# Kernel tuning notes

Measured on AMD Instinct MI355X. Metric: run time of the kernel, lower is better.

## Reference

```python
import jax, jax.numpy as jnp
import numpy as np

D_POINTS, D_MODEL, K, B, N = 64, 128, 16, 2, 16384


def _linear(x, w, b=None):
    y = x @ w.T
    return y if b is None else y + b


def setup_inputs() -> dict:
    key = jax.random.key(0)
    ks = jax.random.split(key, 16)
    s = 0.02
    inp = {
        "new_xyz": jax.random.normal(ks[0], (B, N, 3), jnp.float32),
        "grouped_xyz": jax.random.normal(ks[1], (B, 3, N, K), jnp.float32),
        "grouped_idx": jax.random.randint(ks[2], (B, N, K), 0, N),
        "features": jax.random.normal(ks[3], (B, N, D_POINTS), jnp.float32),
        "fc1_w": jax.random.normal(ks[4], (D_MODEL, D_POINTS), jnp.float32) * s,
        "fc1_b": jnp.zeros((D_MODEL,), jnp.float32),
        "wq": jax.random.normal(ks[5], (D_MODEL, D_MODEL), jnp.float32) * s,
        "wk": jax.random.normal(ks[6], (D_MODEL, D_MODEL), jnp.float32) * s,
        "wv": jax.random.normal(ks[7], (D_MODEL, D_MODEL), jnp.float32) * s,
        "delta_w1": jax.random.normal(ks[8], (D_MODEL, 3), jnp.float32) * s,
        "delta_b1": jnp.zeros((D_MODEL,), jnp.float32),
        "delta_w2": jax.random.normal(ks[9], (D_MODEL, D_MODEL), jnp.float32) * s,
        "delta_b2": jnp.zeros((D_MODEL,), jnp.float32),
        "gamma_w1": jax.random.normal(ks[10], (D_MODEL, D_MODEL), jnp.float32) * s,
        "gamma_b1": jnp.zeros((D_MODEL,), jnp.float32),
        "gamma_w2": jax.random.normal(ks[11], (D_MODEL, D_MODEL), jnp.float32) * s,
        "gamma_b2": jnp.zeros((D_MODEL,), jnp.float32),
    }
    return inp


def reference(new_xyz, grouped_xyz, grouped_idx, features,
              fc1_w, fc1_b, wq, wk, wv,
              delta_w1, delta_b1, delta_w2, delta_b2,
              gamma_w1, gamma_b1, gamma_w2, gamma_b2):
    # x: [B,N,d_model]
    x = _linear(features, fc1_w, fc1_b)
    q = x @ wq.T                               # [B,N,d]
    kx = x @ wk.T                              # [B,N,d]
    vx = x @ wv.T                              # [B,N,d]
    gather = jax.vmap(lambda a, i: a[i])       # per-batch gather -> [B,N,K,d]
    k = gather(kx, grouped_idx)
    v = gather(vx, grouped_idx)
    # pos_enc: fc_delta(new_xyz[:,:,None] - grouped_xyz.permute(0,2,3,1))
    rel = new_xyz[:, :, None, :] - jnp.transpose(grouped_xyz, (0, 2, 3, 1))  # [B,N,K,3]
    pos_enc = _linear(jax.nn.relu(_linear(rel, delta_w1, delta_b1)), delta_w2, delta_b2)
    # attn: fc_gamma(q - k + pos_enc), softmax over neighbor axis
    h = q[:, :, None, :] - k + pos_enc
    attn = _linear(jax.nn.relu(_linear(h, gamma_w1, gamma_b1)), gamma_w2, gamma_b2)
    attn = jax.nn.softmax(attn / np.sqrt(D_MODEL).astype(np.float32), axis=-2)
    out = jnp.einsum('bmnf,bmnf->bmf', attn, v + pos_enc)
    return out
```

## Files before the change

kernel.cpp:

```cpp
#include <hip/hip_runtime.h>
#include <hip/hip_bf16.h>
#include <math.h>

#define BB   2
#define NPTS 16384
#define KNB  16
#define DPTS 64
#define DM   128

typedef float  f32x4  __attribute__((ext_vector_type(4)));
typedef short  bf16x8 __attribute__((ext_vector_type(8)));

__device__ __forceinline__ unsigned short f2bf(float f) {
    union { __hip_bfloat16 h; unsigned short u; } v;
    v.h = __float2bfloat16(f);
    return v.u;
}
__device__ __forceinline__ float bf2f(unsigned short h) {
    union { unsigned u; float f; } v; v.u = ((unsigned)h) << 16;
    return v.f;
}

__device__ __forceinline__ int swz(int row, int col) {
    return row * DM + (col ^ ((row & 7) << 3));
}

#define WOFF_DW2  0
#define WOFF_GW1  16384
#define WOFF_GW2  32768
#define WOFF_WQ   49152
#define WOFF_WK   65536
#define WOFF_WV   81920
#define WOFF_FC1  98304
#define WTOT      106496

__global__ __launch_bounds__(256) void cvtw_kernel(
    const float* __restrict__ dw2, const float* __restrict__ gw1,
    const float* __restrict__ gw2, const float* __restrict__ wq,
    const float* __restrict__ wk, const float* __restrict__ wv,
    const float* __restrict__ fc1_w, unsigned short* __restrict__ wb)
{
    const int i = blockIdx.x * 256 + threadIdx.x;
    if (i >= WTOT) return;
    float v;
    if (i < WOFF_WQ) {
        const int which = i >> 14, off = i & 16383;
        v = (which == 0) ? dw2[off] : (which == 1) ? gw1[off] : gw2[off];
    } else if (i < WOFF_FC1) {
        const int j = i - WOFF_WQ;
        const int which = j >> 14, off = j & 16383;
        v = (which == 0) ? wq[off] : (which == 1) ? wk[off] : wv[off];
    } else {
        v = fc1_w[i - WOFF_FC1];
    }
    wb[i] = f2bf(v);
}

__device__ __forceinline__ void mfma_gemm(const unsigned short* __restrict__ AB,
                                          const unsigned short* __restrict__ Wb,
                                          int lane, int wbase, f32x4 acc[4][2])
{
    const int c = lane & 15, g = lane >> 4;
    bf16x8 Bf[2][4];
#pragma unroll
    for (int ct = 0; ct < 2; ++ct)
#pragma unroll
        for (int ks = 0; ks < 4; ++ks)
            Bf[ct][ks] = *(const bf16x8*)&Wb[(wbase + ct * 16 + c) * DM + ks * 32 + g * 8];
#pragma unroll
    for (int rt = 0; rt < 4; ++rt) {
        bf16x8 Af[4];
#pragma unroll
        for (int ks = 0; ks < 4; ++ks)
            Af[ks] = *(const bf16x8*)&AB[swz(rt * 16 + c, ks * 32 + g * 8)];
#pragma unroll
        for (int ct = 0; ct < 2; ++ct)
#pragma unroll
            for (int ks = 0; ks < 4; ++ks)
                acc[rt][ct] = __builtin_amdgcn_mfma_f32_16x16x32_bf16(
                    Af[ks], Bf[ct][ks], acc[rt][ct], 0, 0, 0);
    }
}

#define P_MT  64
#define FSTR  72

__global__ __launch_bounds__(256, 4) void proj_kernel(
    const float* __restrict__ features, const float* __restrict__ fc1_b,
    const unsigned short* __restrict__ wbf,
    unsigned short* __restrict__ qws, unsigned short* __restrict__ kws,
    unsigned short* __restrict__ vws)
{
    __shared__ __align__(16) unsigned short FB[P_MT * FSTR];
    __shared__ __align__(16) unsigned short XB[P_MT * DM];

    const int tid  = threadIdx.x;
    const int lane = tid & 63;
    const int wave = tid >> 6;
    const int wbase = wave * 32;
    const int c  = lane & 15;
    const int g  = lane >> 4;
    const int g4 = g * 4;
    const size_t gp0 = (size_t)blockIdx.x * P_MT;

    for (int i = tid; i < P_MT * 8; i += 256) {
        const int r = i >> 3, o = i & 7;
        const float4 a = *(const float4*)&features[(gp0 + r) * DPTS + o * 8];
        const float4 b = *(const float4*)&features[(gp0 + r) * DPTS + o * 8 + 4];
        bf16x8 t;
        t[0] = (short)f2bf(a.x); t[1] = (short)f2bf(a.y);
        t[2] = (short)f2bf(a.z); t[3] = (short)f2bf(a.w);
        t[4] = (short)f2bf(b.x); t[5] = (short)f2bf(b.y);
        t[6] = (short)f2bf(b.z); t[7] = (short)f2bf(b.w);
        *(bf16x8*)&FB[r * FSTR + o * 8] = t;
    }
    __syncthreads();

    {
        const unsigned short* fw = wbf + WOFF_FC1;
        const float b0 = fc1_b[wbase + c], b1 = fc1_b[wbase + 16 + c];
        f32x4 acc[4][2];
#pragma unroll
        for (int rt = 0; rt < 4; ++rt) {
            acc[rt][0] = (f32x4)b0;
            acc[rt][1] = (f32x4)b1;
        }
        bf16x8 Bf[2][2];
#pragma unroll
        for (int ct = 0; ct < 2; ++ct)
#pragma unroll
            for (int ks = 0; ks < 2; ++ks)
                Bf[ct][ks] = *(const bf16x8*)&fw[(wbase + ct * 16 + c) * DPTS + ks * 32 + g * 8];
#pragma unroll
        for (int rt = 0; rt < 4; ++rt) {
            bf16x8 Af[2];
#pragma unroll
            for (int ks = 0; ks < 2; ++ks)
                Af[ks] = *(const bf16x8*)&FB[(rt * 16 + c) * FSTR + ks * 32 + g * 8];
#pragma unroll
            for (int ct = 0; ct < 2; ++ct)
#pragma unroll
                for (int ks = 0; ks < 2; ++ks)
                    acc[rt][ct] = __builtin_amdgcn_mfma_f32_16x16x32_bf16(
                        Af[ks], Bf[ct][ks], acc[rt][ct], 0, 0, 0);
        }
#pragma unroll
        for (int ct = 0; ct < 2; ++ct) {
            const int col = wbase + ct * 16 + c;
#pragma unroll
            for (int rt = 0; rt < 4; ++rt)
#pragma unroll
                for (int rg = 0; rg < 4; ++rg)
                    XB[swz(rt * 16 + g4 + rg, col)] = f2bf(acc[rt][ct][rg]);
        }
    }
    __syncthreads();

    const unsigned short* wmat[3] = { wbf + WOFF_WQ, wbf + WOFF_WK, wbf + WOFF_WV };
    unsigned short* outp[3] = { qws, kws, vws };
#pragma unroll
    for (int m = 0; m < 3; ++m) {
        f32x4 acc[4][2];
#pragma unroll
        for (int rt = 0; rt < 4; ++rt)
#pragma unroll
            for (int ct = 0; ct < 2; ++ct) acc[rt][ct] = (f32x4)0.f;
        mfma_gemm(XB, wmat[m], lane, wbase, acc);
#pragma unroll
        for (int ct = 0; ct < 2; ++ct) {
            const int col = wbase + ct * 16 + c;
#pragma unroll
            for (int rt = 0; rt < 4; ++rt)
#pragma unroll
                for (int rg = 0; rg < 4; ++rg)
                    outp[m][(gp0 + rt * 16 + g4 + rg) * DM + col] = f2bf(acc[rt][ct][rg]);
        }
    }
}

#define K2_PTS 4
#define K2_R   (K2_PTS * KNB)

__global__ __launch_bounds__(256, 4) void attn_kernel(
    const float* __restrict__ new_xyz, const float* __restrict__ grouped_xyz,
    const int* __restrict__ grouped_idx,
    const float* __restrict__ dw1, const float* __restrict__ db1,
    const float* __restrict__ db2,
    const float* __restrict__ gb1, const float* __restrict__ gb2,
    const unsigned short* __restrict__ wbf,
    const unsigned short* __restrict__ qws, const unsigned short* __restrict__ kws,
    const unsigned short* __restrict__ vws,
    float* __restrict__ out)
{
    __shared__ __align__(16) unsigned short AB[K2_R * DM];
    __shared__ __align__(16) unsigned short SB[K2_R * DM];
    __shared__ float REL[K2_R * 3];
    __shared__ int   IDX[K2_R];

    const int tid  = threadIdx.x;
    const int lane = tid & 63;
    const int wave = tid >> 6;
    const int wbase = wave * 32;
    const int c  = lane & 15;
    const int g  = lane >> 4;
    const int g4 = g * 4;
    const int rr = tid >> 4;
    const int o8 = (tid & 15) * 8;

    const int b   = blockIdx.x / (NPTS / K2_PTS);
    const int m0  = (blockIdx.x % (NPTS / K2_PTS)) * K2_PTS;
    const size_t gp0 = (size_t)b * NPTS + m0;
    const size_t bN  = (size_t)b * NPTS;
    const float SCL = 0.12751743342f;

    const unsigned short* dw2b = wbf + WOFF_DW2;
    const unsigned short* gw1b = wbf + WOFF_GW1;
    const unsigned short* gw2b = wbf + WOFF_GW2;

    float wr[24], bbv[8];
    {
        const float4* wsrc = (const float4*)&dw1[o8 * 3];
#pragma unroll
        for (int t = 0; t < 6; ++t) ((float4*)wr)[t] = wsrc[t];
        const float4* bsrc = (const float4*)&db1[o8];
        ((float4*)bbv)[0] = bsrc[0];
        ((float4*)bbv)[1] = bsrc[1];
    }

    if (tid < K2_R) {
        const int p = tid >> 4, j = tid & 15;
        const size_t m = gp0 + p;
        const int mi = m0 + p;
        IDX[tid] = grouped_idx[m * KNB + j];
#pragma unroll
        for (int cc = 0; cc < 3; ++cc)
            REL[tid * 3 + cc] = new_xyz[m * 3 + cc]
                              - grouped_xyz[(((size_t)b * 3 + cc) * NPTS + mi) * KNB + j];
    }
    __syncthreads();

    bf16x8 q8[4], k8[4];
#pragma unroll
    for (int it = 0; it < 4; ++it) {
        const int r = it * 16 + rr;
        q8[it] = *(const bf16x8*)&qws[(gp0 + it) * DM + o8];
        k8[it] = *(const bf16x8*)&kws[(bN + IDX[r]) * DM + o8];
    }

#pragma unroll
    for (int it = 0; it < 4; ++it) {
        const int r = it * 16 + rr;
        const float rx = REL[r * 3 + 0], ry = REL[r * 3 + 1], rz = REL[r * 3 + 2];
        bf16x8 t;
#pragma unroll
        for (int j = 0; j < 8; ++j) {
            float v = bbv[j];
            v = fmaf(rx, wr[j * 3 + 0], v);
            v = fmaf(ry, wr[j * 3 + 1], v);
            v = fmaf(rz, wr[j * 3 + 2], v);
            t[j] = (short)f2bf(fmaxf(v, 0.f));
        }
        *(bf16x8*)&AB[swz(r, o8)] = t;
    }
    __syncthreads();

    f32x4 posr[4][2];
    {
        const float b0 = db2[wbase + c], b1 = db2[wbase + 16 + c];
#pragma unroll
        for (int rt = 0; rt < 4; ++rt) {
            posr[rt][0] = (f32x4)b0;
            posr[rt][1] = (f32x4)b1;
        }
        mfma_gemm(AB, dw2b, lane, wbase, posr);
#pragma unroll
        for (int ct = 0; ct < 2; ++ct) {
            const int col = wbase + ct * 16 + c;
#pragma unroll
            for (int rt = 0; rt < 4; ++rt)
#pragma unroll
                for (int rg = 0; rg < 4; ++rg)
                    SB[swz(rt * 16 + g4 + rg, col)] = f2bf(posr[rt][ct][rg]);
        }
    }
    __syncthreads();

#pragma unroll
    for (int it = 0; it < 4; ++it) {
        const int r = it * 16 + rr;
        const bf16x8 p8 = *(const bf16x8*)&SB[swz(r, o8)];
        bf16x8 t;
#pragma unroll
        for (int j = 0; j < 8; ++j) {
            const float hv = bf2f((unsigned short)q8[it][j])
                           - bf2f((unsigned short)k8[it][j])
                           + bf2f((unsigned short)p8[j]);
            t[j] = (short)f2bf(hv);
        }
        *(bf16x8*)&AB[swz(r, o8)] = t;
    }
    __syncthreads();

    {
        f32x4 acc[4][2];
        const float b0 = gb1[wbase + c], b1 = gb1[wbase + 16 + c];
#pragma unroll
        for (int rt = 0; rt < 4; ++rt) {
            acc[rt][0] = (f32x4)b0;
            acc[rt][1] = (f32x4)b1;
        }
        mfma_gemm(AB, gw1b, lane, wbase, acc);
#pragma unroll
        for (int ct = 0; ct < 2; ++ct) {
            const int col = wbase + ct * 16 + c;
#pragma unroll
            for (int rt = 0; rt < 4; ++rt)
#pragma unroll
                for (int rg = 0; rg < 4; ++rg)
                    SB[swz(rt * 16 + g4 + rg, col)] = f2bf(fmaxf(acc[rt][ct][rg], 0.f));
        }
    }
    __syncthreads();

    f32x4 lg[4][2];
#pragma unroll
    for (int rt = 0; rt < 4; ++rt)
#pragma unroll
        for (int ct = 0; ct < 2; ++ct) lg[rt][ct] = (f32x4)0.f;
    mfma_gemm(SB, gw2b, lane, wbase, lg);
#pragma unroll
    for (int ct = 0; ct < 2; ++ct) {
        const int col = wbase + ct * 16 + c;
        const float bb = gb2[col];
#pragma unroll
        for (int rt = 0; rt < 4; ++rt)
#pragma unroll
            for (int rg = 0; rg < 4; ++rg)
                lg[rt][ct][rg] = (lg[rt][ct][rg] + bb) * SCL;
    }

#pragma unroll
    for (int rt = 0; rt < 4; ++rt)
#pragma unroll
    for (int ct = 0; ct < 2; ++ct) {
        const int col = wbase + ct * 16 + c;
        f32x4 l = lg[rt][ct];
        float mx = fmaxf(fmaxf(l[0], l[1]), fmaxf(l[2], l[3]));
        mx = fmaxf(mx, __shfl_xor(mx, 16));
        mx = fmaxf(mx, __shfl_xor(mx, 32));
        f32x4 e;
        e[0] = __builtin_amdgcn_exp2f(l[0] - mx);
        e[1] = __builtin_amdgcn_exp2f(l[1] - mx);
        e[2] = __builtin_amdgcn_exp2f(l[2] - mx);
        e[3] = __builtin_amdgcn_exp2f(l[3] - mx);
        float s = e[0] + e[1] + e[2] + e[3];
        s += __shfl_xor(s, 16);
        s += __shfl_xor(s, 32);
        float o = 0.f;
#pragma unroll
        for (int rg = 0; rg < 4; ++rg) {
            const int row = rt * 16 + g4 + rg;
            const float vv = bf2f(vws[(bN + IDX[row]) * DM + col]) + posr[rt][ct][rg];
            o = fmaf(e[rg], vv, o);
        }
        o += __shfl_xor(o, 16);
        o += __shfl_xor(o, 32);
        if (g == 0)
            out[(gp0 + rt) * DM + col] = o * __builtin_amdgcn_rcpf(s);
    }
}

extern "C" void kernel_launch(void* const* d_in, const int* in_sizes, int n_in,
                              void* d_out, int out_size, void* d_ws, size_t ws_size,
                              hipStream_t stream)
{
    const float* new_xyz     = (const float*)d_in[0];
    const float* grouped_xyz = (const float*)d_in[1];
    const int*   grouped_idx = (const int*)d_in[2];
    const float* features    = (const float*)d_in[3];
    const float* fc1_w = (const float*)d_in[4];
    const float* fc1_b = (const float*)d_in[5];
    const float* wq    = (const float*)d_in[6];
    const float* wk    = (const float*)d_in[7];
    const float* wv    = (const float*)d_in[8];
    const float* dw1   = (const float*)d_in[9];
    const float* db1   = (const float*)d_in[10];
    const float* dw2   = (const float*)d_in[11];
    const float* db2   = (const float*)d_in[12];
    const float* gw1   = (const float*)d_in[13];
    const float* gb1   = (const float*)d_in[14];
    const float* gw2   = (const float*)d_in[15];
    const float* gb2   = (const float*)d_in[16];
    float* out = (float*)d_out;

    unsigned short* ws = (unsigned short*)d_ws;
    const size_t npt = (size_t)BB * NPTS * DM;
    unsigned short* qws = ws;
    unsigned short* kws = ws + npt;
    unsigned short* vws = ws + 2 * npt;
    unsigned short* wbf = ws + 3 * npt;

    cvtw_kernel<<<(WTOT + 255) / 256, 256, 0, stream>>>(
        dw2, gw1, gw2, wq, wk, wv, fc1_w, wbf);

    proj_kernel<<<(BB * NPTS) / P_MT, 256, 0, stream>>>(
        features, fc1_b, wbf, qws, kws, vws);

    attn_kernel<<<(BB * NPTS) / K2_PTS, 256, 0, stream>>>(
        new_xyz, grouped_xyz, grouped_idx,
        dw1, db1, db2, gb1, gb2,
        wbf, qws, kws, vws, out);
}
```

Before: 163.0 us.

## Interleave K/V rows and share one LDS buffer to raise attention occupancy

K and V projections are now stored interleaved per point (row stride 2*DM), so the gathered K and V rows for a neighbor index sit next to each other in memory and may share cache lines and DRAM pages. The attention kernel folds its two 16KB LDS staging buffers into one, adding extra barriers before each in-place overwrite. Launch bounds are raised from 4 to 8 blocks per SM to allow more concurrent blocks. The tighter bound may force register spilling, and the added syncs serialize the GEMM phases more.

```diff
diff --git a/kernel.cpp b/kernel.cpp
--- a/kernel.cpp
+++ b/kernel.cpp
@@ -88,8 +88,7 @@
 __global__ __launch_bounds__(256, 4) void proj_kernel(
     const float* __restrict__ features, const float* __restrict__ fc1_b,
     const unsigned short* __restrict__ wbf,
-    unsigned short* __restrict__ qws, unsigned short* __restrict__ kws,
-    unsigned short* __restrict__ vws)
+    unsigned short* __restrict__ qws, unsigned short* __restrict__ kvws)
 {
     __shared__ __align__(16) unsigned short FB[P_MT * FSTR];
     __shared__ __align__(16) unsigned short XB[P_MT * DM];
@@ -157,7 +156,6 @@
     __syncthreads();
 
     const unsigned short* wmat[3] = { wbf + WOFF_WQ, wbf + WOFF_WK, wbf + WOFF_WV };
-    unsigned short* outp[3] = { qws, kws, vws };
 #pragma unroll
     for (int m = 0; m < 3; ++m) {
         f32x4 acc[4][2];
@@ -172,8 +170,13 @@
 #pragma unroll
             for (int rt = 0; rt < 4; ++rt)
 #pragma unroll
-                for (int rg = 0; rg < 4; ++rg)
-                    outp[m][(gp0 + rt * 16 + g4 + rg) * DM + col] = f2bf(acc[rt][ct][rg]);
+                for (int rg = 0; rg < 4; ++rg) {
+                    const size_t row = gp0 + rt * 16 + g4 + rg;
+                    unsigned short* dst = (m == 0)
+                        ? &qws[row * DM + col]
+                        : &kvws[row * (2 * DM) + (m == 2 ? DM : 0) + col];
+                    *dst = f2bf(acc[rt][ct][rg]);
+                }
         }
     }
 }
@@ -181,19 +184,17 @@
 #define K2_PTS 4
 #define K2_R   (K2_PTS * KNB)
 
-__global__ __launch_bounds__(256, 4) void attn_kernel(
+__global__ __launch_bounds__(256, 8) void attn_kernel(
     const float* __restrict__ new_xyz, const float* __restrict__ grouped_xyz,
     const int* __restrict__ grouped_idx,
     const float* __restrict__ dw1, const float* __restrict__ db1,
     const float* __restrict__ db2,
     const float* __restrict__ gb1, const float* __restrict__ gb2,
     const unsigned short* __restrict__ wbf,
-    const unsigned short* __restrict__ qws, const unsigned short* __restrict__ kws,
-    const unsigned short* __restrict__ vws,
+    const unsigned short* __restrict__ qws, const unsigned short* __restrict__ kvws,
     float* __restrict__ out)
 {
-    __shared__ __align__(16) unsigned short AB[K2_R * DM];
-    __shared__ __align__(16) unsigned short SB[K2_R * DM];
+    __shared__ __align__(16) unsigned short X[K2_R * DM];
     __shared__ float REL[K2_R * 3];
     __shared__ int   IDX[K2_R];
 
@@ -244,7 +245,7 @@
     for (int it = 0; it < 4; ++it) {
         const int r = it * 16 + rr;
         q8[it] = *(const bf16x8*)&qws[(gp0 + it) * DM + o8];
-        k8[it] = *(const bf16x8*)&kws[(bN + IDX[r]) * DM + o8];
+        k8[it] = *(const bf16x8*)&kvws[(bN + IDX[r]) * (2 * DM) + o8];
     }
 
 #pragma unroll
@@ -260,7 +261,7 @@
             v = fmaf(rz, wr[j * 3 + 2], v);
             t[j] = (short)f2bf(fmaxf(v, 0.f));
         }
-        *(bf16x8*)&AB[swz(r, o8)] = t;
+        *(bf16x8*)&X[swz(r, o8)] = t;
     }
     __syncthreads();
 
@@ -272,23 +273,24 @@
             posr[rt][0] = (f32x4)b0;
             posr[rt][1] = (f32x4)b1;
         }
-        mfma_gemm(AB, dw2b, lane, wbase, posr);
-#pragma unroll
-        for (int ct = 0; ct < 2; ++ct) {
-            const int col = wbase + ct * 16 + c;
-#pragma unroll
-            for (int rt = 0; rt < 4; ++rt)
-#pragma unroll
-                for (int rg = 0; rg < 4; ++rg)
-                    SB[swz(rt * 16 + g4 + rg, col)] = f2bf(posr[rt][ct][rg]);
-        }
+    }
+    mfma_gemm(X, dw2b, lane, wbase, posr);
+    __syncthreads();
+#pragma unroll
+    for (int ct = 0; ct < 2; ++ct) {
+        const int col = wbase + ct * 16 + c;
+#pragma unroll
+        for (int rt = 0; rt < 4; ++rt)
+#pragma unroll
+            for (int rg = 0; rg < 4; ++rg)
+                X[swz(rt * 16 + g4 + rg, col)] = f2bf(posr[rt][ct][rg]);
     }
     __syncthreads();
 
 #pragma unroll
     for (int it = 0; it < 4; ++it) {
         const int r = it * 16 + rr;
-        const bf16x8 p8 = *(const bf16x8*)&SB[swz(r, o8)];
+        const bf16x8 p8 = *(const bf16x8*)&X[swz(r, o8)];
         bf16x8 t;
 #pragma unroll
         for (int j = 0; j < 8; ++j) {
@@ -297,7 +299,7 @@
                            + bf2f((unsigned short)p8[j]);
             t[j] = (short)f2bf(hv);
         }
-        *(bf16x8*)&AB[swz(r, o8)] = t;
+        *(bf16x8*)&X[swz(r, o8)] = t;
     }
     __syncthreads();
 
@@ -309,7 +311,8 @@
             acc[rt][0] = (f32x4)b0;
             acc[rt][1] = (f32x4)b1;
         }
-        mfma_gemm(AB, gw1b, lane, wbase, acc);
+        mfma_gemm(X, gw1b, lane, wbase, acc);
+        __syncthreads();
 #pragma unroll
         for (int ct = 0; ct < 2; ++ct) {
             const int col = wbase + ct * 16 + c;
@@ -317,7 +320,7 @@
             for (int rt = 0; rt < 4; ++rt)
 #pragma unroll
                 for (int rg = 0; rg < 4; ++rg)
-                    SB[swz(rt * 16 + g4 + rg, col)] = f2bf(fmaxf(acc[rt][ct][rg], 0.f));
+                    X[swz(rt * 16 + g4 + rg, col)] = f2bf(fmaxf(acc[rt][ct][rg], 0.f));
         }
     }
     __syncthreads();
@@ -327,7 +330,7 @@
     for (int rt = 0; rt < 4; ++rt)
 #pragma unroll
         for (int ct = 0; ct < 2; ++ct) lg[rt][ct] = (f32x4)0.f;
-    mfma_gemm(SB, gw2b, lane, wbase, lg);
+    mfma_gemm(X, gw2b, lane, wbase, lg);
 #pragma unroll
     for (int ct = 0; ct < 2; ++ct) {
         const int col = wbase + ct * 16 + c;
@@ -360,7 +363,8 @@
 #pragma unroll
         for (int rg = 0; rg < 4; ++rg) {
             const int row = rt * 16 + g4 + rg;
-            const float vv = bf2f(vws[(bN + IDX[row]) * DM + col]) + posr[rt][ct][rg];
+            const float vv = bf2f(kvws[(bN + IDX[row]) * (2 * DM) + DM + col])
+                           + posr[rt][ct][rg];
             o = fmaf(e[rg], vv, o);
         }
         o += __shfl_xor(o, 16);
@@ -395,19 +399,18 @@
 
     unsigned short* ws = (unsigned short*)d_ws;
     const size_t npt = (size_t)BB * NPTS * DM;
-    unsigned short* qws = ws;
-    unsigned short* kws = ws + npt;
-    unsigned short* vws = ws + 2 * npt;
-    unsigned short* wbf = ws + 3 * npt;
+    unsigned short* qws  = ws;
+    unsigned short* kvws = ws + npt;
+    unsigned short* wbf  = ws + 3 * npt;
 
     cvtw_kernel<<<(WTOT + 255) / 256, 256, 0, stream>>>(
         dw2, gw1, gw2, wq, wk, wv, fc1_w, wbf);
 
     proj_kernel<<<(BB * NPTS) / P_MT, 256, 0, stream>>>(
-        features, fc1_b, wbf, qws, kws, vws);
+        features, fc1_b, wbf, qws, kvws);
 
     attn_kernel<<<(BB * NPTS) / K2_PTS, 256, 0, stream>>>(
         new_xyz, grouped_xyz, grouped_idx,
         dw1, db1, db2, gb1, gb2,
-        wbf, qws, kws, vws, out);
-}
+        wbf, qws, kvws, out);
+}
```

Result: slower. 353.6 us (+116.9%).

## Stage v+pos in LDS via coalesced gather, drop register-held pos_enc

Applied to the files above, without the earlier changes.

Replaces the scattered per-element 2-byte global loads of the gathered v rows in the softmax epilogue with coalesced 16-byte row loads issued early. v + pos_enc is computed in bf16 and kept in a new LDS buffer. The posr accumulator no longer stays live across the gamma GEMMs, which lowers register pressure. A single buffer is reused for the GEMM inputs and outputs, so extra barriers are added, and v+pos_enc is now rounded to bf16 before the weighted sum.

```diff
diff --git a/kernel.cpp b/kernel.cpp
--- a/kernel.cpp
+++ b/kernel.cpp
@@ -192,8 +192,8 @@
     const unsigned short* __restrict__ vws,
     float* __restrict__ out)
 {
-    __shared__ __align__(16) unsigned short AB[K2_R * DM];
-    __shared__ __align__(16) unsigned short SB[K2_R * DM];
+    __shared__ __align__(16) unsigned short X[K2_R * DM];
+    __shared__ __align__(16) unsigned short VB[K2_R * DM];
     __shared__ float REL[K2_R * 3];
     __shared__ int   IDX[K2_R];
 
@@ -260,19 +260,20 @@
             v = fmaf(rz, wr[j * 3 + 2], v);
             t[j] = (short)f2bf(fmaxf(v, 0.f));
         }
-        *(bf16x8*)&AB[swz(r, o8)] = t;
-    }
-    __syncthreads();
-
-    f32x4 posr[4][2];
+        *(bf16x8*)&X[swz(r, o8)] = t;
+    }
+    __syncthreads();
+
     {
+        f32x4 acc[4][2];
         const float b0 = db2[wbase + c], b1 = db2[wbase + 16 + c];
 #pragma unroll
         for (int rt = 0; rt < 4; ++rt) {
-            posr[rt][0] = (f32x4)b0;
-            posr[rt][1] = (f32x4)b1;
-        }
-        mfma_gemm(AB, dw2b, lane, wbase, posr);
+            acc[rt][0] = (f32x4)b0;
+            acc[rt][1] = (f32x4)b1;
+        }
+        mfma_gemm(X, dw2b, lane, wbase, acc);
+        __syncthreads();
 #pragma unroll
         for (int ct = 0; ct < 2; ++ct) {
             const int col = wbase + ct * 16 + c;
@@ -280,24 +281,31 @@
             for (int rt = 0; rt < 4; ++rt)
 #pragma unroll
                 for (int rg = 0; rg < 4; ++rg)
-                    SB[swz(rt * 16 + g4 + rg, col)] = f2bf(posr[rt][ct][rg]);
-        }
-    }
+                    X[swz(rt * 16 + g4 + rg, col)] = f2bf(acc[rt][ct][rg]);
+        }
+    }
+
+    bf16x8 v8[4];
+#pragma unroll
+    for (int it = 0; it < 4; ++it)
+        v8[it] = *(const bf16x8*)&vws[(bN + IDX[it * 16 + rr]) * DM + o8];
     __syncthreads();
 
 #pragma unroll
     for (int it = 0; it < 4; ++it) {
         const int r = it * 16 + rr;
-        const bf16x8 p8 = *(const bf16x8*)&SB[swz(r, o8)];
-        bf16x8 t;
+        const bf16x8 p8 = *(const bf16x8*)&X[swz(r, o8)];
+        bf16x8 t, vp;
 #pragma unroll
         for (int j = 0; j < 8; ++j) {
+            const float pv = bf2f((unsigned short)p8[j]);
             const float hv = bf2f((unsigned short)q8[it][j])
-                           - bf2f((unsigned short)k8[it][j])
-                           + bf2f((unsigned short)p8[j]);
-            t[j] = (short)f2bf(hv);
-        }
-        *(bf16x8*)&AB[swz(r, o8)] = t;
+                           - bf2f((unsigned short)k8[it][j]) + pv;
+            t[j]  = (short)f2bf(hv);
+            vp[j] = (short)f2bf(bf2f((unsigned short)v8[it][j]) + pv);
+        }
+        *(bf16x8*)&X[swz(r, o8)]  = t;
+        *(bf16x8*)&VB[swz(r, o8)] = vp;
     }
     __syncthreads();
 
@@ -309,7 +317,8 @@
             acc[rt][0] = (f32x4)b0;
             acc[rt][1] = (f32x4)b1;
         }
-        mfma_gemm(AB, gw1b, lane, wbase, acc);
+        mfma_gemm(X, gw1b, lane, wbase, acc);
+        __syncthreads();
 #pragma unroll
         for (int ct = 0; ct < 2; ++ct) {
             const int col = wbase + ct * 16 + c;
@@ -317,7 +326,7 @@
             for (int rt = 0; rt < 4; ++rt)
 #pragma unroll
                 for (int rg = 0; rg < 4; ++rg)
-                    SB[swz(rt * 16 + g4 + rg, col)] = f2bf(fmaxf(acc[rt][ct][rg], 0.f));
+                    X[swz(rt * 16 + g4 + rg, col)] = f2bf(fmaxf(acc[rt][ct][rg], 0.f));
         }
     }
     __syncthreads();
@@ -327,7 +336,7 @@
     for (int rt = 0; rt < 4; ++rt)
 #pragma unroll
         for (int ct = 0; ct < 2; ++ct) lg[rt][ct] = (f32x4)0.f;
-    mfma_gemm(SB, gw2b, lane, wbase, lg);
+    mfma_gemm(X, gw2b, lane, wbase, lg);
 #pragma unroll
     for (int ct = 0; ct < 2; ++ct) {
         const int col = wbase + ct * 16 + c;
@@ -360,7 +369,7 @@
 #pragma unroll
         for (int rg = 0; rg < 4; ++rg) {
             const int row = rt * 16 + g4 + rg;
-            const float vv = bf2f(vws[(bN + IDX[row]) * DM + col]) + posr[rt][ct][rg];
+            const float vv = bf2f(VB[swz(row, col)]);
             o = fmaf(e[rg], vv, o);
         }
         o += __shfl_xor(o, 16);
```

Result: faster. 159.7 us (-2.1%).
